# Performance work log

Measured on AMD Instinct MI355X. Metric: run time of the kernel, lower is better.

The kernel has to match this reference:

```python
import jax, jax.numpy as jnp
import numpy as np
from jax import lax

NUM_GROUPS = 16
GN_EPS = 1e-5
POOL = 4
CLAMP_MIN, CLAMP_MAX = 0.0, 1.0


def setup_inputs() -> dict:
    key = jax.random.key(0)
    ks = jax.random.split(key, 4)
    x = jax.random.normal(ks[0], (128, 8, 128, 128), dtype=jnp.float32)
    conv_weight = jax.random.normal(ks[1], (64, 8, 3, 3), dtype=jnp.float32) * 0.1
    conv_bias = jax.random.normal(ks[2], (64,), dtype=jnp.float32) * 0.1
    gn_weight = jnp.ones((64,), dtype=jnp.float32)
    gn_bias = jnp.zeros((64,), dtype=jnp.float32)
    scale = jax.random.normal(ks[3], (64, 1, 1), dtype=jnp.float32)
    return {"x": x, "conv_weight": conv_weight, "conv_bias": conv_bias,
            "gn_weight": gn_weight, "gn_bias": gn_bias, "scale": scale}


def reference(x, conv_weight, conv_bias, gn_weight, gn_bias, scale):
    # Conv2d (stride=1, padding=0)
    y = lax.conv_general_dilated(
        x, conv_weight, window_strides=(1, 1), padding='VALID',
        dimension_numbers=('NCHW', 'OIHW', 'NCHW'))
    y = y + conv_bias[None, :, None, None]  # [B, C, H, W] = [128, 64, 126, 126]

    # GroupNorm over (channels-in-group, H, W) per sample
    B, C, H, W = y.shape
    yg = y.reshape(B, NUM_GROUPS, C // NUM_GROUPS, H, W)
    mean = jnp.mean(yg, axis=(2, 3, 4), keepdims=True)
    var = jnp.var(yg, axis=(2, 3, 4), keepdims=True)
    yn = ((yg - mean) * lax.rsqrt(var + GN_EPS)).reshape(B, C, H, W)
    yn = yn * gn_weight[None, :, None, None] + gn_bias[None, :, None, None]

    # scale (broadcast [C,1,1])
    yn = yn * scale[None]

    # MaxPool2d(kernel=4, stride=4)
    p = lax.reduce_window(yn, -jnp.inf, lax.max,
                          window_dimensions=(1, 1, POOL, POOL),
                          window_strides=(1, 1, POOL, POOL),
                          padding='VALID')  # [128, 64, 31, 31]

    # clamp
    return jnp.clip(p, CLAMP_MIN, CLAMP_MAX)
```

## Files before the change

### kernel.cpp

```cpp
#include <hip/hip_runtime.h>
#include <math.h>

typedef _Float16 f16x8 __attribute__((ext_vector_type(8)));
typedef float f32x4 __attribute__((ext_vector_type(4)));

#define CIN 8
#define HIN 128
#define WIN 128
#define OH 126
#define OW 126
#define COUT 64
#define NB 128
#define NGROUPS 16
#define CPG 4
#define PWN 31
#define XROWS 34

#define NPOOL (NB*PWN*PWN*COUT)
#define OFF_PART (NPOOL/2)
#define NPART (NB*NGROUPS*16*2)

__global__ __launch_bounds__(256) __attribute__((amdgpu_waves_per_eu(4, 4)))
void conv_mfma_kernel(const float* __restrict__ x,
                      const float* __restrict__ w,
                      const float* __restrict__ bias,
                      const float* __restrict__ gnw,
                      const float* __restrict__ scale,
                      float* __restrict__ ws)
{
  __shared__ __align__(16) _Float16 xs[XROWS*34*8];
  __shared__ __align__(16) _Float16 wls[9*64*8];
  __shared__ float red[4][16][2];

  const int tid  = threadIdx.x;
  const int lane = tid & 63, wave = tid >> 6;
  const int tileIdx = blockIdx.x;
  const int tx = tileIdx & 3, ty = tileIdx >> 2;
  const int b  = blockIdx.y;
  const int ox0 = tx*32, oy0 = ty*32;

  for (int idx = tid; idx < 9*64*8; idx += 256) {
    const int ci = idx & 7, n = (idx >> 3) & 63, khw = idx >> 9;
    wls[idx] = (_Float16)w[(n*CIN + ci)*9 + khw];
  }

  const float* xb = x + (size_t)b * CIN*HIN*WIN;
  for (int p = tid; p < XROWS*34; p += 256) {
    const int r = p / 34, c = p - r*34;
    const int iy = oy0 + r, ix = ox0 + c;
    const bool ok = (iy < HIN) && (ix < WIN);
    const int gbase = iy*WIN + ix;
    f16x8 pk;
    #pragma unroll
    for (int ci = 0; ci < 8; ++ci) {
      const float v = ok ? xb[ci*HIN*WIN + gbase] : 0.f;
      pk[ci] = (_Float16)v;
    }
    *(f16x8*)&xs[p*8] = pk;
  }
  __syncthreads();

  const int q = lane >> 4, ln = lane & 15;

  f16x8 bf[4][3];
  #pragma unroll
  for (int nt = 0; nt < 4; ++nt) {
    #pragma unroll
    for (int c = 0; c < 2; ++c)
      bf[nt][c] = *(const f16x8*)&wls[((c*4 + q)*64 + nt*16 + ln)*8];
    if (q == 0)
      bf[nt][2] = *(const f16x8*)&wls[((8)*64 + nt*16 + ln)*8];
    else
      bf[nt][2] = (f16x8){0,0,0,0,0,0,0,0};
  }

  const int dy = ln >> 2, dx = ln & 3;
  int aoff[3];
  #pragma unroll
  for (int c = 0; c < 3; ++c) {
    const int khw = c*4 + q;
    const int ky = khw / 3, kx = khw - 3*(khw/3);
    aoff[c] = (khw < 9) ? ((dy + ky)*34 + (dx + kx))*8 : 0;
  }

  float bias_r[4], sgn[4];
  #pragma unroll
  for (int nt = 0; nt < 4; ++nt) {
    const int c = nt*16 + ln;
    bias_r[nt] = bias[c];
    sgn[nt] = (gnw[c]*scale[c] >= 0.f) ? 1.f : -1.f;
  }

  float s[4]  = {0.f,0.f,0.f,0.f};
  float sq[4] = {0.f,0.f,0.f,0.f};
  _Float16* wext = (_Float16*)ws;

  #pragma unroll 2
  for (int i = 0; i < 16; ++i) {
    const int wyl = wave*2 + (i >> 3), wxl = i & 7;
    const int base = (wyl*4*34 + wxl*4)*8;

    f32x4 acc[4];
    #pragma unroll
    for (int nt = 0; nt < 4; ++nt) {
      const float bv = bias_r[nt];
      acc[nt] = (f32x4){bv, bv, bv, bv};
    }
    #pragma unroll
    for (int c = 0; c < 3; ++c) {
      const f16x8 a = *(const f16x8*)&xs[base + aoff[c]];
      #pragma unroll
      for (int nt = 0; nt < 4; ++nt)
        acc[nt] = __builtin_amdgcn_mfma_f32_16x16x32_f16(a, bf[nt][c], acc[nt], 0, 0, 0);
    }

    const int wyg = ty*8 + wyl, wxg = tx*8 + wxl;
    if ((wyg < PWN) && (wxg < PWN)) {
      const size_t rowbase = ((size_t)(b*PWN + wyg)*PWN + wxg)*COUT;
      float m4[4];
      #pragma unroll
      for (int nt = 0; nt < 4; ++nt) {
        const float v0 = acc[nt][0], v1 = acc[nt][1];
        const float v2 = acc[nt][2], v3 = acc[nt][3];
        s[nt]  += (v0+v1) + (v2+v3);
        sq[nt] += v0*v0 + v1*v1 + v2*v2 + v3*v3;
        const float sg = sgn[nt];
        float m = fmaxf(fmaxf(sg*v0, sg*v1), fmaxf(sg*v2, sg*v3));
        m = fmaxf(m, __shfl_xor(m, 16, 64));
        m = fmaxf(m, __shfl_xor(m, 32, 64));
        m4[nt] = sg*m;
      }
      float mv = m4[0];
      mv = (q == 1) ? m4[1] : mv;
      mv = (q == 2) ? m4[2] : mv;
      mv = (q == 3) ? m4[3] : mv;
      wext[rowbase + lane] = (_Float16)mv;
    } else {
      const bool yv = (wyg*4 + q) < OH;
      #pragma unroll
      for (int nt = 0; nt < 4; ++nt) {
        #pragma unroll
        for (int r = 0; r < 4; ++r) {
          const bool okp = yv && (wxg*4 + r < OW);
          const float v = okp ? acc[nt][r] : 0.f;
          s[nt] += v; sq[nt] += v*v;
        }
      }
    }
  }

  #pragma unroll
  for (int nt = 0; nt < 4; ++nt) {
    float a = s[nt], c2 = sq[nt];
    a  += __shfl_xor(a, 16, 64);  a  += __shfl_xor(a, 32, 64);
    a  += __shfl_xor(a, 1, 64);   a  += __shfl_xor(a, 2, 64);
    c2 += __shfl_xor(c2, 16, 64); c2 += __shfl_xor(c2, 32, 64);
    c2 += __shfl_xor(c2, 1, 64);  c2 += __shfl_xor(c2, 2, 64);
    if (lane < 16 && (lane & 3) == 0) {
      red[wave][nt*4 + (ln >> 2)][0] = a;
      red[wave][nt*4 + (ln >> 2)][1] = c2;
    }
  }
  __syncthreads();
  if (tid < 32) {
    const int g = tid >> 1, k = tid & 1;
    const float t = red[0][g][k] + red[1][g][k] + red[2][g][k] + red[3][g][k];
    ws[OFF_PART + (((size_t)b*NGROUPS + g)*16 + tileIdx)*2 + k] = t;
  }
}

__global__ __launch_bounds__(256)
void tail_kernel(const float* __restrict__ gnw,
                 const float* __restrict__ gnb,
                 const float* __restrict__ scale,
                 const float* __restrict__ ws,
                 float* __restrict__ out)
{
  __shared__ float stat[NGROUPS*2];
  __shared__ float AB[128];
  __shared__ float vout[COUT*PWN];

  const int tid = threadIdx.x;
  const int xb  = blockIdx.x;
  const int b   = blockIdx.y;

  if (tid < 32) {
    const int g = tid >> 1, k = tid & 1;
    const float* p = ws + OFF_PART + (size_t)(b*NGROUPS + g)*32 + k;
    float a = 0.f;
    #pragma unroll
    for (int t = 0; t < 16; ++t) a += p[t*2];
    stat[g*2 + k] = a;
  }
  __syncthreads();
  if (tid < COUT) {
    const int c = tid, g = c >> 2;
    const float N = (float)(CPG * OH * OW);
    const float mean = stat[g*2] / N;
    const float var  = stat[g*2 + 1] / N - mean*mean;
    const float inv  = rsqrtf(var + 1e-5f);
    const float ag   = inv * gnw[c];
    AB[c]      = ag * scale[c];
    AB[64 + c] = (gnb[c] - mean * ag) * scale[c];
  }
  __syncthreads();

  const _Float16* wext = (const _Float16*)ws;
  #pragma unroll
  for (int r = 0; r < 2; ++r) {
    const int wy = xb*2 + r;
    if (wy >= PWN) break;
    const size_t rb = (size_t)(b*PWN + wy)*PWN*COUT;

    if (tid < 248) {
      const f16x8 e = *(const f16x8*)&wext[rb + tid*8];
      const int wx = tid >> 3, c0 = (tid & 7)*8;
      #pragma unroll
      for (int j = 0; j < 8; ++j) {
        const int c = c0 + j;
        float v = fmaf(AB[c], (float)e[j], AB[64 + c]);
        v = fminf(fmaxf(v, 0.f), 1.f);
        vout[c*PWN + wx] = v;
      }
    }
    __syncthreads();
    for (int e = tid; e < COUT*PWN; e += 256) {
      const int c = e / PWN, wx = e - c*PWN;
      out[(((size_t)b*COUT + c)*PWN + wy)*PWN + wx] = vout[e];
    }
    __syncthreads();
  }
}

extern "C" void kernel_launch(void* const* d_in, const int* in_sizes, int n_in,
                              void* d_out, int out_size, void* d_ws, size_t ws_size,
                              hipStream_t stream)
{
  const float* x     = (const float*)d_in[0];
  const float* cw    = (const float*)d_in[1];
  const float* cb    = (const float*)d_in[2];
  const float* gnw   = (const float*)d_in[3];
  const float* gnb   = (const float*)d_in[4];
  const float* scale = (const float*)d_in[5];
  float* out = (float*)d_out;
  float* ws  = (float*)d_ws;

  dim3 gridA(16, NB, 1);
  conv_mfma_kernel<<<gridA, 256, 0, stream>>>(x, cw, cb, gnw, scale, ws);

  dim3 gridT(16, NB, 1);
  tail_kernel<<<gridT, 256, 0, stream>>>(gnw, gnb, scale, ws, out);
}
```

Before: 184.2 us.

## Remap MFMA tile to 1x16 output rows and pool across row iterations

Each MFMA A-tile now covers 16 consecutive output pixels along one row rather than a 4x4 patch. Max-pooling becomes a per-lane running max over four row iterations, which removes the cross-lane shuffles. Pooled results are staged through a small shared buffer so each wave writes them with wider 8-byte stores. It also drops the waves_per_eu attribute and trims edge handling, at the cost of an LDS round trip and a different LDS read pattern.

After: 192.3 us. +4.4%, slower.

```diff
diff --git a/kernel.cpp b/kernel.cpp
--- a/kernel.cpp
+++ b/kernel.cpp
@@ -18,9 +18,8 @@
 
 #define NPOOL (NB*PWN*PWN*COUT)
 #define OFF_PART (NPOOL/2)
-#define NPART (NB*NGROUPS*16*2)
-
-__global__ __launch_bounds__(256) __attribute__((amdgpu_waves_per_eu(4, 4)))
+
+__global__ __launch_bounds__(256)
 void conv_mfma_kernel(const float* __restrict__ x,
                       const float* __restrict__ w,
                       const float* __restrict__ bias,
@@ -30,6 +29,7 @@
 {
   __shared__ __align__(16) _Float16 xs[XROWS*34*8];
   __shared__ __align__(16) _Float16 wls[9*64*8];
+  __shared__ __align__(8)  _Float16 sbuf[4][256];
   __shared__ float red[4][16][2];
 
   const int tid  = threadIdx.x;
@@ -74,13 +74,12 @@
       bf[nt][2] = (f16x8){0,0,0,0,0,0,0,0};
   }
 
-  const int dy = ln >> 2, dx = ln & 3;
   int aoff[3];
   #pragma unroll
   for (int c = 0; c < 3; ++c) {
     const int khw = c*4 + q;
     const int ky = khw / 3, kx = khw - 3*(khw/3);
-    aoff[c] = (khw < 9) ? ((dy + ky)*34 + (dx + kx))*8 : 0;
+    aoff[c] = (khw < 9) ? (ky*34 + kx + ln)*8 : ln*8;
   }
 
   float bias_r[4], sgn[4];
@@ -95,56 +94,58 @@
   float sq[4] = {0.f,0.f,0.f,0.f};
   _Float16* wext = (_Float16*)ws;
 
-  #pragma unroll 2
-  for (int i = 0; i < 16; ++i) {
-    const int wyl = wave*2 + (i >> 3), wxl = i & 7;
-    const int base = (wyl*4*34 + wxl*4)*8;
-
-    f32x4 acc[4];
-    #pragma unroll
-    for (int nt = 0; nt < 4; ++nt) {
-      const float bv = bias_r[nt];
-      acc[nt] = (f32x4){bv, bv, bv, bv};
-    }
-    #pragma unroll
-    for (int c = 0; c < 3; ++c) {
-      const f16x8 a = *(const f16x8*)&xs[base + aoff[c]];
-      #pragma unroll
-      for (int nt = 0; nt < 4; ++nt)
-        acc[nt] = __builtin_amdgcn_mfma_f32_16x16x32_f16(a, bf[nt][c], acc[nt], 0, 0, 0);
-    }
-
-    const int wyg = ty*8 + wyl, wxg = tx*8 + wxl;
-    if ((wyg < PWN) && (wxg < PWN)) {
-      const size_t rowbase = ((size_t)(b*PWN + wyg)*PWN + wxg)*COUT;
-      float m4[4];
+  const float xm_hi = (q < 3) ? 1.f : 0.f;
+
+  for (int bd = 0; bd < 4; ++bd) {
+    const int wy_l = wave*2 + (bd >> 1);
+    const int x0   = (bd & 1) << 4;
+    const int wy_g = ty*8 + wy_l;
+    const bool xedge = (tx == 3) && (x0 == 16);
+
+    float mx[4] = {-1e30f, -1e30f, -1e30f, -1e30f};
+
+    #pragma unroll
+    for (int sy = 0; sy < 4; ++sy) {
+      const int y_l = wy_l*4 + sy;
+      if (oy0 + y_l >= OH) break;
+      const int base = (y_l*34 + x0)*8;
+
+      f32x4 acc[4];
       #pragma unroll
       for (int nt = 0; nt < 4; ++nt) {
-        const float v0 = acc[nt][0], v1 = acc[nt][1];
-        const float v2 = acc[nt][2], v3 = acc[nt][3];
+        const float bv = bias_r[nt];
+        acc[nt] = (f32x4){bv, bv, bv, bv};
+      }
+      #pragma unroll
+      for (int c = 0; c < 3; ++c) {
+        const f16x8 a = *(const f16x8*)&xs[base + aoff[c]];
+        #pragma unroll
+        for (int nt = 0; nt < 4; ++nt)
+          acc[nt] = __builtin_amdgcn_mfma_f32_16x16x32_f16(a, bf[nt][c], acc[nt], 0, 0, 0);
+      }
+
+      #pragma unroll
+      for (int nt = 0; nt < 4; ++nt) {
+        float v0 = acc[nt][0], v1 = acc[nt][1];
+        float v2 = acc[nt][2], v3 = acc[nt][3];
+        if (xedge) { v2 *= xm_hi; v3 *= xm_hi; }
         s[nt]  += (v0+v1) + (v2+v3);
         sq[nt] += v0*v0 + v1*v1 + v2*v2 + v3*v3;
         const float sg = sgn[nt];
-        float m = fmaxf(fmaxf(sg*v0, sg*v1), fmaxf(sg*v2, sg*v3));
-        m = fmaxf(m, __shfl_xor(m, 16, 64));
-        m = fmaxf(m, __shfl_xor(m, 32, 64));
-        m4[nt] = sg*m;
-      }
-      float mv = m4[0];
-      mv = (q == 1) ? m4[1] : mv;
-      mv = (q == 2) ? m4[2] : mv;
-      mv = (q == 3) ? m4[3] : mv;
-      wext[rowbase + lane] = (_Float16)mv;
-    } else {
-      const bool yv = (wyg*4 + q) < OH;
-      #pragma unroll
-      for (int nt = 0; nt < 4; ++nt) {
-        #pragma unroll
-        for (int r = 0; r < 4; ++r) {
-          const bool okp = yv && (wxg*4 + r < OW);
-          const float v = okp ? acc[nt][r] : 0.f;
-          s[nt] += v; sq[nt] += v*v;
-        }
+        const float m = fmaxf(fmaxf(sg*v0, sg*v1), fmaxf(sg*v2, sg*v3));
+        mx[nt] = fmaxf(mx[nt], m);
+      }
+    }
+
+    if (wy_g < PWN) {
+      #pragma unroll
+      for (int nt = 0; nt < 4; ++nt)
+        sbuf[wave][q*64 + nt*16 + ln] = (_Float16)(sgn[nt]*mx[nt]);
+      const int nw = xedge ? 3 : 4;
+      if (lane < nw*16) {
+        const int wx0_g = tx*8 + (x0 >> 2);
+        const uint2 v = *(const uint2*)&sbuf[wave][lane*4];
+        *(uint2*)&wext[(((size_t)b*PWN + wy_g)*PWN + wx0_g)*COUT + lane*4] = v;
       }
     }
   }
```

## Pre-pack input to padded fp16 NHWC and double-buffer tiles via direct-to-LDS loads

Applied to the files above, without the earlier changes.

Adds a pre-pass kernel that converts x into a zero-padded fp16 channel-interleaved layout in workspace. The conv kernel then uses 512-thread blocks that sweep four vertical tiles, loading each next tile with global_load_lds into a second LDS buffer while MFMA work runs on the current one. The aim is to hide input load latency and drop the per-element conversion and strided gathers from the conv kernel. In exchange it adds an extra kernel launch and a full write and re-read of a half-size copy of x, and cuts the conv grid from 16x128 blocks to 4x128 blocks.

Measured after the change: 177.0 us. 3.9% less time.

```diff
diff --git a/kernel.cpp b/kernel.cpp
--- a/kernel.cpp
+++ b/kernel.cpp
@@ -15,12 +15,200 @@
 #define CPG 4
 #define PWN 31
 #define XROWS 34
+#define XH_DIM 130
+#define TPIX (34*34)
+
+#define XH_BYTES   ((size_t)NB*XH_DIM*XH_DIM*CIN*2)
+#define WEXT_BYTES ((size_t)NB*PWN*PWN*COUT*2)
+#define PART_BYTES ((size_t)NB*NGROUPS*4*2*4)
+#define WS_NEEDED  (XH_BYTES + WEXT_BYTES + PART_BYTES)
 
 #define NPOOL (NB*PWN*PWN*COUT)
-#define OFF_PART (NPOOL/2)
-#define NPART (NB*NGROUPS*16*2)
-
-__global__ __launch_bounds__(256) __attribute__((amdgpu_waves_per_eu(4, 4)))
+#define OFF_PART_OLD (NPOOL/2)
+
+__global__ __launch_bounds__(192)
+void xpack_kernel(const float* __restrict__ x, _Float16* __restrict__ xh)
+{
+  const int iy = blockIdx.x;
+  const int b  = blockIdx.y;
+  const int ix = threadIdx.x;
+  if (ix >= XH_DIM) return;
+  f16x8 pk = {0,0,0,0,0,0,0,0};
+  if (iy < HIN && ix < WIN) {
+    const float* xb = x + (size_t)b*CIN*HIN*WIN + iy*WIN + ix;
+    #pragma unroll
+    for (int ci = 0; ci < 8; ++ci)
+      pk[ci] = (_Float16)xb[ci*HIN*WIN];
+  }
+  *(f16x8*)&xh[(((size_t)b*XH_DIM + iy)*XH_DIM + ix)*CIN] = pk;
+}
+
+__global__ __launch_bounds__(512)
+void conv_dma_kernel(const _Float16* __restrict__ xh,
+                     const float* __restrict__ w,
+                     const float* __restrict__ bias,
+                     const float* __restrict__ gnw,
+                     const float* __restrict__ scale,
+                     _Float16* __restrict__ wext,
+                     float* __restrict__ parts)
+{
+  __shared__ __align__(16) _Float16 xs[2][TPIX*8];
+  __shared__ __align__(16) _Float16 wls[9*64*8];
+  __shared__ float red[8][16][2];
+
+  const int tid  = threadIdx.x;
+  const int lane = tid & 63, wave = tid >> 6;
+  const int tx = blockIdx.x;
+  const int b  = blockIdx.y;
+  const int ox0 = tx*32;
+
+  for (int idx = tid; idx < 9*64*8; idx += 512) {
+    const int ci = idx & 7, n = (idx >> 3) & 63, khw = idx >> 9;
+    wls[idx] = (_Float16)w[(n*CIN + ci)*9 + khw];
+  }
+
+  const int q = lane >> 4, ln = lane & 15;
+
+  auto stage = [&](int buf, int ty) {
+    const int oy0 = ty*32;
+    #pragma unroll
+    for (int k = 0; k < 3; ++k) {
+      const int p = k*512 + tid;
+      if (p < TPIX) {
+        const int r = p / 34, c = p - r*34;
+        const size_t gb = (((size_t)b*XH_DIM + (oy0 + r))*XH_DIM + (ox0 + c))*CIN;
+        __builtin_amdgcn_global_load_lds(
+            (const __attribute__((address_space(1))) void*)(xh + gb),
+            (__attribute__((address_space(3))) void*)&xs[buf][p*8],
+            16, 0, 0);
+      }
+    }
+  };
+
+  stage(0, 0);
+
+  asm volatile("s_waitcnt vmcnt(0)" ::: "memory");
+  __syncthreads();
+
+  f16x8 bf[4][3];
+  #pragma unroll
+  for (int nt = 0; nt < 4; ++nt) {
+    #pragma unroll
+    for (int c = 0; c < 2; ++c)
+      bf[nt][c] = *(const f16x8*)&wls[((c*4 + q)*64 + nt*16 + ln)*8];
+    if (q == 0)
+      bf[nt][2] = *(const f16x8*)&wls[((8)*64 + nt*16 + ln)*8];
+    else
+      bf[nt][2] = (f16x8){0,0,0,0,0,0,0,0};
+  }
+
+  const int dy = ln >> 2, dx = ln & 3;
+  int aoff[3];
+  #pragma unroll
+  for (int c = 0; c < 3; ++c) {
+    const int khw = c*4 + q;
+    const int ky = khw / 3, kx = khw - 3*(khw/3);
+    aoff[c] = (khw < 9) ? ((dy + ky)*34 + (dx + kx))*8 : 0;
+  }
+
+  float bias_r[4], sgn[4];
+  #pragma unroll
+  for (int nt = 0; nt < 4; ++nt) {
+    const int c = nt*16 + ln;
+    bias_r[nt] = bias[c];
+    sgn[nt] = (gnw[c]*scale[c] >= 0.f) ? 1.f : -1.f;
+  }
+
+  float s[4]  = {0.f,0.f,0.f,0.f};
+  float sq[4] = {0.f,0.f,0.f,0.f};
+
+  for (int ty = 0; ty < 4; ++ty) {
+    const int cur = ty & 1;
+    if (ty < 3) stage(cur ^ 1, ty + 1);
+
+    #pragma unroll 2
+    for (int i = 0; i < 8; ++i) {
+      const int wxl = i;
+      const int base = (wave*4*34 + wxl*4)*8;
+
+      f32x4 acc[4];
+      #pragma unroll
+      for (int nt = 0; nt < 4; ++nt) {
+        const float bv = bias_r[nt];
+        acc[nt] = (f32x4){bv, bv, bv, bv};
+      }
+      #pragma unroll
+      for (int c = 0; c < 3; ++c) {
+        const f16x8 a = *(const f16x8*)&xs[cur][base + aoff[c]];
+        #pragma unroll
+        for (int nt = 0; nt < 4; ++nt)
+          acc[nt] = __builtin_amdgcn_mfma_f32_16x16x32_f16(a, bf[nt][c], acc[nt], 0, 0, 0);
+      }
+
+      const int wyg = ty*8 + wave, wxg = tx*8 + wxl;
+      if ((wyg < PWN) && (wxg < PWN)) {
+        const size_t rowbase = ((size_t)(b*PWN + wyg)*PWN + wxg)*COUT;
+        float m4[4];
+        #pragma unroll
+        for (int nt = 0; nt < 4; ++nt) {
+          const float v0 = acc[nt][0], v1 = acc[nt][1];
+          const float v2 = acc[nt][2], v3 = acc[nt][3];
+          s[nt]  += (v0+v1) + (v2+v3);
+          sq[nt] += v0*v0 + v1*v1 + v2*v2 + v3*v3;
+          const float sg = sgn[nt];
+          float m = fmaxf(fmaxf(sg*v0, sg*v1), fmaxf(sg*v2, sg*v3));
+          m = fmaxf(m, __shfl_xor(m, 16, 64));
+          m = fmaxf(m, __shfl_xor(m, 32, 64));
+          m4[nt] = sg*m;
+        }
+        float mv = m4[0];
+        mv = (q == 1) ? m4[1] : mv;
+        mv = (q == 2) ? m4[2] : mv;
+        mv = (q == 3) ? m4[3] : mv;
+        wext[rowbase + lane] = (_Float16)mv;
+      } else {
+        const bool yv = (wyg*4 + q) < OH;
+        #pragma unroll
+        for (int nt = 0; nt < 4; ++nt) {
+          #pragma unroll
+          for (int r = 0; r < 4; ++r) {
+            const bool okp = yv && (wxg*4 + r < OW);
+            const float v = okp ? acc[nt][r] : 0.f;
+            s[nt] += v; sq[nt] += v*v;
+          }
+        }
+      }
+    }
+
+    if (ty < 3) {
+      asm volatile("s_waitcnt vmcnt(0)" ::: "memory");
+      __syncthreads();
+    }
+  }
+
+  #pragma unroll
+  for (int nt = 0; nt < 4; ++nt) {
+    float a = s[nt], c2 = sq[nt];
+    a  += __shfl_xor(a, 16, 64);  a  += __shfl_xor(a, 32, 64);
+    a  += __shfl_xor(a, 1, 64);   a  += __shfl_xor(a, 2, 64);
+    c2 += __shfl_xor(c2, 16, 64); c2 += __shfl_xor(c2, 32, 64);
+    c2 += __shfl_xor(c2, 1, 64);  c2 += __shfl_xor(c2, 2, 64);
+    if (lane < 16 && (lane & 3) == 0) {
+      red[wave][nt*4 + (ln >> 2)][0] = a;
+      red[wave][nt*4 + (ln >> 2)][1] = c2;
+    }
+  }
+  __syncthreads();
+  if (tid < 32) {
+    const int g = tid >> 1, k = tid & 1;
+    float t = 0.f;
+    #pragma unroll
+    for (int wv = 0; wv < 8; ++wv) t += red[wv][g][k];
+    parts[(((size_t)b*NGROUPS + g)*4 + tx)*2 + k] = t;
+  }
+}
+
+__global__ __launch_bounds__(256)
 void conv_mfma_kernel(const float* __restrict__ x,
                       const float* __restrict__ w,
                       const float* __restrict__ bias,
@@ -43,7 +231,6 @@
     const int ci = idx & 7, n = (idx >> 3) & 63, khw = idx >> 9;
     wls[idx] = (_Float16)w[(n*CIN + ci)*9 + khw];
   }
-
   const float* xb = x + (size_t)b * CIN*HIN*WIN;
   for (int p = tid; p < XROWS*34; p += 256) {
     const int r = p / 34, c = p - r*34;
@@ -61,19 +248,15 @@
   __syncthreads();
 
   const int q = lane >> 4, ln = lane & 15;
-
   f16x8 bf[4][3];
   #pragma unroll
   for (int nt = 0; nt < 4; ++nt) {
     #pragma unroll
     for (int c = 0; c < 2; ++c)
       bf[nt][c] = *(const f16x8*)&wls[((c*4 + q)*64 + nt*16 + ln)*8];
-    if (q == 0)
-      bf[nt][2] = *(const f16x8*)&wls[((8)*64 + nt*16 + ln)*8];
-    else
-      bf[nt][2] = (f16x8){0,0,0,0,0,0,0,0};
-  }
-
+    if (q == 0) bf[nt][2] = *(const f16x8*)&wls[((8)*64 + nt*16 + ln)*8];
+    else        bf[nt][2] = (f16x8){0,0,0,0,0,0,0,0};
+  }
   const int dy = ln >> 2, dx = ln & 3;
   int aoff[3];
   #pragma unroll
@@ -82,7 +265,6 @@
     const int ky = khw / 3, kx = khw - 3*(khw/3);
     aoff[c] = (khw < 9) ? ((dy + ky)*34 + (dx + kx))*8 : 0;
   }
-
   float bias_r[4], sgn[4];
   #pragma unroll
   for (int nt = 0; nt < 4; ++nt) {
@@ -90,7 +272,6 @@
     bias_r[nt] = bias[c];
     sgn[nt] = (gnw[c]*scale[c] >= 0.f) ? 1.f : -1.f;
   }
-
   float s[4]  = {0.f,0.f,0.f,0.f};
   float sq[4] = {0.f,0.f,0.f,0.f};
   _Float16* wext = (_Float16*)ws;
@@ -99,7 +280,6 @@
   for (int i = 0; i < 16; ++i) {
     const int wyl = wave*2 + (i >> 3), wxl = i & 7;
     const int base = (wyl*4*34 + wxl*4)*8;
-
     f32x4 acc[4];
     #pragma unroll
     for (int nt = 0; nt < 4; ++nt) {
@@ -113,7 +293,6 @@
       for (int nt = 0; nt < 4; ++nt)
         acc[nt] = __builtin_amdgcn_mfma_f32_16x16x32_f16(a, bf[nt][c], acc[nt], 0, 0, 0);
     }
-
     const int wyg = ty*8 + wyl, wxg = tx*8 + wxl;
     if ((wyg < PWN) && (wxg < PWN)) {
       const size_t rowbase = ((size_t)(b*PWN + wyg)*PWN + wxg)*COUT;
@@ -148,7 +327,6 @@
       }
     }
   }
-
   #pragma unroll
   for (int nt = 0; nt < 4; ++nt) {
     float a = s[nt], c2 = sq[nt];
@@ -165,7 +343,7 @@
   if (tid < 32) {
     const int g = tid >> 1, k = tid & 1;
     const float t = red[0][g][k] + red[1][g][k] + red[2][g][k] + red[3][g][k];
-    ws[OFF_PART + (((size_t)b*NGROUPS + g)*16 + tileIdx)*2 + k] = t;
+    ws[OFF_PART_OLD + (((size_t)b*NGROUPS + g)*16 + tileIdx)*2 + k] = t;
   }
 }
 
@@ -173,7 +351,9 @@
 void tail_kernel(const float* __restrict__ gnw,
                  const float* __restrict__ gnb,
                  const float* __restrict__ scale,
-                 const float* __restrict__ ws,
+                 const _Float16* __restrict__ wext,
+                 const float* __restrict__ parts,
+                 const int nparts,
                  float* __restrict__ out)
 {
   __shared__ float stat[NGROUPS*2];
@@ -186,10 +366,9 @@
 
   if (tid < 32) {
     const int g = tid >> 1, k = tid & 1;
-    const float* p = ws + OFF_PART + (size_t)(b*NGROUPS + g)*32 + k;
+    const float* p = parts + ((size_t)(b*NGROUPS + g)*nparts)*2 + k;
     float a = 0.f;
-    #pragma unroll
-    for (int t = 0; t < 16; ++t) a += p[t*2];
+    for (int t = 0; t < nparts; ++t) a += p[t*2];
     stat[g*2 + k] = a;
   }
   __syncthreads();
@@ -205,7 +384,6 @@
   }
   __syncthreads();
 
-  const _Float16* wext = (const _Float16*)ws;
   #pragma unroll
   for (int r = 0; r < 2; ++r) {
     const int wy = xb*2 + r;
@@ -245,9 +423,18 @@
   float* out = (float*)d_out;
   float* ws  = (float*)d_ws;
 
-  dim3 gridA(16, NB, 1);
-  conv_mfma_kernel<<<gridA, 256, 0, stream>>>(x, cw, cb, gnw, scale, ws);
-
-  dim3 gridT(16, NB, 1);
-  tail_kernel<<<gridT, 256, 0, stream>>>(gnw, gnb, scale, ws, out);
+  if (ws_size >= WS_NEEDED) {
+    _Float16* xh   = (_Float16*)ws;
+    _Float16* wext = (_Float16*)((char*)ws + XH_BYTES);
+    float*    prt  = (float*)((char*)ws + XH_BYTES + WEXT_BYTES);
+
+    xpack_kernel<<<dim3(XH_DIM, NB), 192, 0, stream>>>(x, xh);
+    conv_dma_kernel<<<dim3(4, NB), 512, 0, stream>>>(xh, cw, cb, gnw, scale, wext, prt);
+    tail_kernel<<<dim3(16, NB), 256, 0, stream>>>(gnw, gnb, scale, wext, prt, 4, out);
+  } else {
+    conv_mfma_kernel<<<dim3(16, NB), 256, 0, stream>>>(x, cw, cb, gnw, scale, ws);
+    tail_kernel<<<dim3(16, NB), 256, 0, stream>>>(gnw, gnb, scale,
+                                                  (const _Float16*)ws,
+                                                  ws + OFF_PART_OLD, 16, out);
+  }
 }
```
